# Kernel optimization log

Measured on AMD Instinct MI355X. Metric: run time of the kernel, lower is better.

## Reference

```python
import jax, jax.numpy as jnp
import numpy as np

B, NU, IN, H, VD = 4096, 6, 600, 600, 400
KD_IN, NH_IN = 64, 1
KD_C, NH_C = 32, 4
K = 4


def setup_inputs() -> dict:
    key = jax.random.key(0)
    ks = jax.random.split(key, 12)
    f = jax.random.normal
    return dict(
        x=f(ks[0], (B, 1, IN), jnp.float32),
        hs=f(ks[1], (B, NU, H), jnp.float32),
        cs=f(ks[2], (B, NU, H), jnp.float32),
        Wk=f(ks[3], (IN, NH_IN * KD_IN), jnp.float32) * 0.02,   # input-attn key Linear (no bias)
        Wv=f(ks[4], (IN, NH_IN * VD), jnp.float32) * 0.02,      # input-attn value Linear (no bias)
        Wq=f(ks[5], (NU, H, NH_IN * KD_IN), jnp.float32) * 0.01,  # GroupLinear query
        Wi2h=f(ks[6], (NU, VD, 4 * H), jnp.float32) * 0.01,     # GroupLSTMCell i2h
        Wh2h=f(ks[7], (NU, H, 4 * H), jnp.float32) * 0.01,      # GroupLSTMCell h2h
        Wck=f(ks[8], (NU, H, NH_C * KD_C), jnp.float32) * 0.01,  # comm key GroupLinear
        Wcq=f(ks[9], (NU, H, NH_C * KD_C), jnp.float32) * 0.01,  # comm query GroupLinear
        Wcv=f(ks[10], (NU, H, NH_C * H), jnp.float32) * 0.01,   # comm value GroupLinear
        Wco=f(ks[11], (NU, NH_C * H, H), jnp.float32) * 0.01,   # comm output_fc GroupLinear
    )


def _heads(t, nh, d):
    # (B, N, nh*d) -> (B, nh, N, d)
    b, n, _ = t.shape
    return t.reshape(b, n, nh, d).transpose(0, 2, 1, 3)


def reference(x, hs, cs, Wk, Wv, Wq, Wi2h, Wh2h, Wck, Wcq, Wcv, Wco):
    b = x.shape[0]
    # append null input along key axis -> (B, 2, IN)
    xcat = jnp.concatenate([x, jnp.zeros((b, 1, IN), x.dtype)], axis=1)

    # ---- input attention + top-k unit mask ----
    key = _heads(xcat @ Wk, NH_IN, KD_IN)                 # (B, nh, 2, kd)
    val = _heads(xcat @ Wv, NH_IN, VD).mean(axis=1)       # (B, 2, vd) (mean over heads)
    qry = _heads(jnp.einsum('buh,uhk->buk', hs, Wq), NH_IN, KD_IN)  # (B, nh, NU, kd)
    scores = jnp.einsum('bhuk,bhmk->bhum', qry, key) / jnp.sqrt(jnp.asarray(KD_IN, x.dtype))
    scores = scores.mean(axis=1)                          # (B, NU, 2)
    idx = jax.lax.top_k(scores[:, :, 0], K)[1]            # (B, K) active units
    mask = jnp.zeros((b, NU), x.dtype).at[jnp.arange(b)[:, None], idx].set(1.0)
    probs = jax.nn.softmax(scores, axis=-1)               # (dropout p is identity in eval)
    inputs = jnp.einsum('bum,bmv->buv', probs, val) * mask[:, :, None]  # (B, NU, vd)

    # ---- grouped LSTM cell ----
    preact = (jnp.einsum('buv,uvo->buo', inputs, Wi2h)
              + jnp.einsum('buh,uho->buo', hs, Wh2h))     # (B, NU, 4H)
    gates = jax.nn.sigmoid(preact[:, :, :3 * H])
    g_t = jnp.tanh(preact[:, :, 3 * H:])
    i_t = gates[:, :, :H]
    f_t = gates[:, :, H:2 * H]
    o_t = gates[:, :, 2 * H:]
    c_t = cs * f_t + i_t * g_t
    h_t = o_t * jnp.tanh(c_t)

    # ---- blocked_grad: identity fwd, grad*mask bwd ----
    m3 = mask[:, :, None]
    h_b = h_t * m3 + jax.lax.stop_gradient(h_t * (1.0 - m3))

    # ---- masked communication attention ----
    ck = _heads(jnp.einsum('buh,uhk->buk', h_b, Wck), NH_C, KD_C)  # (B, nh, NU, kd)
    cq = _heads(jnp.einsum('buh,uhk->buk', h_b, Wcq), NH_C, KD_C)
    cv = _heads(jnp.einsum('buh,uhk->buk', h_b, Wcv), NH_C, H)     # (B, nh, NU, H)
    cscores = jnp.einsum('bhuk,bhmk->bhum', cq, ck) / jnp.sqrt(jnp.asarray(KD_C, x.dtype))
    cprobs = jax.nn.softmax(cscores, axis=-1) * mask[:, None, :, None]  # mask query rows
    ctx = jnp.einsum('bhum,bhmd->bhud', cprobs, cv)       # (B, nh, NU, H)
    ctx = ctx.transpose(0, 2, 1, 3).reshape(b, NU, NH_C * H)
    ctx = jnp.einsum('buf,ufo->buo', ctx, Wco)            # (B, NU, H)
    h_new = ctx + h_b

    # ---- keep inactive units' old state ----
    hs_out = m3 * h_new + (1.0 - m3) * hs
    cs_out = m3 * c_t + (1.0 - m3) * cs
    return hs_out, cs_out
```

## Files before the change

kernel.cpp:

```cpp
#include <hip/hip_runtime.h>
#include <cstdint>
#include <cstddef>


typedef _Float16 f16;
typedef _Float16 f16x8 __attribute__((ext_vector_type(8)));
typedef float    f32x4 __attribute__((ext_vector_type(4)));

__device__ __forceinline__ void async16(const void* g, void* l) {
    __builtin_amdgcn_global_load_lds((const __attribute__((address_space(1))) void*)g,
                                     (__attribute__((address_space(3))) void*)l,
                                     16, 0, 0);
}

template <typename CT, int BN, int WM, int WN>
__global__ __launch_bounds__(512, 2)
void mfma_gemm2(const f16* __restrict__ A, const f16* __restrict__ W,
                CT* __restrict__ C, int K, int lda, int ldc, int Nreal,
                long sAu, long sWu, long sCu)
{
    constexpr int MI = 256 / WM / 16;
    const int gx = gridDim.x, gy = gridDim.y;
    int bid = blockIdx.x + gx * (blockIdx.y + gy * blockIdx.z);
    const int nwg = gx * gy * gridDim.z;
    if ((nwg & 7) == 0)
        bid = (bid & 7) * (nwg >> 3) + (bid >> 3);
    const int bx  = bid % gx;
    const int byz = bid / gx;
    const int by  = byz % gy;
    const int bz  = byz / gy;
    A += (long)bz * sAu;
    W += (long)bz * sWu;
    C += (long)bz * sCu;
    const int tm = bx * 256;
    const int tn = by * BN;

    __shared__ __attribute__((aligned(16))) f16 As[2][256 * 64];
    __shared__ __attribute__((aligned(16))) f16 Ws[2][BN * 64];

    const int tid  = threadIdx.x;
    const int wave = tid >> 6;
    const int lane = tid & 63;
    const int wm = (wave / WN) * (256 / WM);
    const int wn = (wave % WN) * (BN / WN);
    const int srow = lane >> 3;
    const int scol = ((lane & 7) ^ srow) * 8;
    const int mrow = lane & 15;
    const int kq   = (lane >> 4) * 8;
    const int swz  = (mrow & 7) << 3;

    f32x4 acc[MI][4] = {};

    auto stage = [&](int b, int kk) {
#pragma unroll
        for (int t = 0; t < 4; t++) {
            const int rb = t * 64 + wave * 8;
            async16(A + (long)(tm + rb + srow) * lda + (kk + scol), &As[b][rb * 64]);
        }
#pragma unroll
        for (int t = 0; t < BN / 64; t++) {
            const int rb = t * 64 + wave * 8;
            async16(W + (long)(tn + rb + srow) * K + (kk + scol), &Ws[b][rb * 64]);
        }
    };
    auto compute = [&](int b) {
#pragma unroll
        for (int c = 0; c < 2; c++) {
            const int cc = (c * 32 + kq) ^ swz;
            f16x8 aF[MI], wF[4];
#pragma unroll
            for (int i = 0; i < MI; i++)
                aF[i] = *(const f16x8*)&As[b][(wm + i * 16 + mrow) * 64 + cc];
#pragma unroll
            for (int j = 0; j < 4; j++)
                wF[j] = *(const f16x8*)&Ws[b][(wn + j * 16 + mrow) * 64 + cc];
#pragma unroll
            for (int i = 0; i < MI; i++)
#pragma unroll
                for (int j = 0; j < 4; j++)
                    acc[i][j] = __builtin_amdgcn_mfma_f32_16x16x32_f16(aF[i], wF[j], acc[i][j], 0, 0, 0);
        }
    };

    stage(0, 0);
    int bsel = 0;
    const int nk = K >> 6;
    for (int s = 0; s < nk; s++) {
        __syncthreads();
        if (s + 1 < nk) stage(bsel ^ 1, (s + 1) << 6);
        compute(bsel);
        bsel ^= 1;
    }
    const int rrow = (lane >> 4) * 4;
#pragma unroll
    for (int i = 0; i < MI; i++)
#pragma unroll
        for (int j = 0; j < 4; j++) {
            const int col = tn + wn + j * 16 + mrow;
            if (col < Nreal)
#pragma unroll
                for (int r = 0; r < 4; r++)
                    C[(long)(tm + wm + i * 16 + rrow + r) * ldc + col] = (CT)acc[i][j][r];
        }
}

template <typename CT>
__global__ __launch_bounds__(256)
void mfma_gemm(const f16* __restrict__ A, const f16* __restrict__ W,
               CT* __restrict__ C, int K, int lda, int ldc,
               long sAu, long sWu, long sCu)
{
    A += (long)blockIdx.z * sAu;
    W += (long)blockIdx.z * sWu;
    C += (long)blockIdx.z * sCu;
    const int tm = blockIdx.x * 128;
    const int tn = blockIdx.y * 128;
    __shared__ __attribute__((aligned(16))) f16 As[2][128 * 64];
    __shared__ __attribute__((aligned(16))) f16 Ws[2][128 * 64];
    const int tid  = threadIdx.x;
    const int wave = tid >> 6;
    const int lane = tid & 63;
    const int wm = (wave >> 1) * 64;
    const int wn = (wave & 1) * 64;
    const int srow = lane >> 3;
    const int scol = ((lane & 7) ^ srow) * 8;
    const int mrow = lane & 15;
    const int kq   = (lane >> 4) * 8;
    const int swz  = (mrow & 7) << 3;

    f32x4 acc[4][4] = {};

    auto stage = [&](int b, int kk) {
#pragma unroll
        for (int t = 0; t < 4; t++) {
            const int rbase = t * 32 + wave * 8;
            async16(A + (long)(tm + rbase + srow) * lda + (kk + scol), &As[b][rbase * 64]);
            async16(W + (long)(tn + rbase + srow) * K   + (kk + scol), &Ws[b][rbase * 64]);
        }
    };
    auto compute = [&](int b) {
#pragma unroll
        for (int c = 0; c < 2; c++) {
            const int cc = (c * 32 + kq) ^ swz;
            f16x8 aF[4], wF[4];
#pragma unroll
            for (int i = 0; i < 4; i++)
                aF[i] = *(const f16x8*)&As[b][(wm + i * 16 + mrow) * 64 + cc];
#pragma unroll
            for (int j = 0; j < 4; j++)
                wF[j] = *(const f16x8*)&Ws[b][(wn + j * 16 + mrow) * 64 + cc];
#pragma unroll
            for (int i = 0; i < 4; i++)
#pragma unroll
                for (int j = 0; j < 4; j++)
                    acc[i][j] = __builtin_amdgcn_mfma_f32_16x16x32_f16(aF[i], wF[j], acc[i][j], 0, 0, 0);
        }
    };

    stage(0, 0);
    int bsel = 0;
    const int nk = K >> 6;
    for (int s = 0; s < nk; s++) {
        __syncthreads();
        if (s + 1 < nk) stage(bsel ^ 1, (s + 1) << 6);
        compute(bsel);
        bsel ^= 1;
    }
    const int rrow = (lane >> 4) * 4;
#pragma unroll
    for (int i = 0; i < 4; i++)
#pragma unroll
        for (int j = 0; j < 4; j++)
#pragma unroll
            for (int r = 0; r < 4; r++)
                C[(long)(tm + wm + i * 16 + rrow + r) * ldc + (tn + wn + j * 16 + mrow)] = (CT)acc[i][j][r];
}

__global__ __launch_bounds__(256)
void sgemm_fused(const float* __restrict__ hs, const float* __restrict__ Wq,
                 const float* __restrict__ x, const float* __restrict__ Wk,
                 float* __restrict__ q, float* __restrict__ kx)
{
    const int z = blockIdx.z;
    const float* A; const float* W; float* C; int lda, ldc;
    if (z < 6) { A = hs + z * 600; W = Wq + (long)z * 38400; C = q + z * 64; lda = 3600; ldc = 384; }
    else       { A = x;            W = Wk;                   C = kx;         lda = 600;  ldc = 64;  }
    const int K = 600;
    const int tm = blockIdx.x * 64;
    __shared__ __attribute__((aligned(16))) float AsT[16][64];
    __shared__ __attribute__((aligned(16))) float Ws[16][64];
    const int t = threadIdx.x;
    const int arow = t >> 2, akc = (t & 3) * 4;
    const int wkw = t >> 4, wn = (t & 15) * 4;
    const int tx = t & 15, ty = t >> 4;

    float4 aR, wR;
    const float* Arow = A + (long)(tm + arow) * lda;
    auto loadA = [&](int kk) {
        const int k0 = kk + akc;
        const float* p = Arow + k0;
        if (k0 + 3 < K) aR = *(const float4*)p;
        else {
            aR.x = (k0 + 0 < K) ? p[0] : 0.f; aR.y = (k0 + 1 < K) ? p[1] : 0.f;
            aR.z = (k0 + 2 < K) ? p[2] : 0.f; aR.w = (k0 + 3 < K) ? p[3] : 0.f;
        }
    };
    auto loadW = [&](int kk) {
        const int k = kk + wkw;
        if (k < K) wR = *(const float4*)(W + (long)k * 64 + wn);
        else       wR = float4{0.f, 0.f, 0.f, 0.f};
    };
    loadA(0); loadW(0);
    float acc[4][4] = {{0.f}};
    const int NS = 38;
    for (int s = 0; s < NS; s++) {
        __syncthreads();
        AsT[akc + 0][arow] = aR.x; AsT[akc + 1][arow] = aR.y;
        AsT[akc + 2][arow] = aR.z; AsT[akc + 3][arow] = aR.w;
        *(float4*)&Ws[wkw][wn] = wR;
        __syncthreads();
        if (s + 1 < NS) { loadA((s + 1) * 16); loadW((s + 1) * 16); }
#pragma unroll
        for (int k = 0; k < 16; k++) {
            const float4 av = *(const float4*)&AsT[k][ty * 4];
            const float4 wv = *(const float4*)&Ws[k][tx * 4];
            acc[0][0] += av.x * wv.x; acc[0][1] += av.x * wv.y; acc[0][2] += av.x * wv.z; acc[0][3] += av.x * wv.w;
            acc[1][0] += av.y * wv.x; acc[1][1] += av.y * wv.y; acc[1][2] += av.y * wv.z; acc[1][3] += av.y * wv.w;
            acc[2][0] += av.z * wv.x; acc[2][1] += av.z * wv.y; acc[2][2] += av.z * wv.z; acc[2][3] += av.z * wv.w;
            acc[3][0] += av.w * wv.x; acc[3][1] += av.w * wv.y; acc[3][2] += av.w * wv.z; acc[3][3] += av.w * wv.w;
        }
    }
#pragma unroll
    for (int r = 0; r < 4; r++)
#pragma unroll
        for (int c = 0; c < 4; c++)
            C[(long)(tm + ty * 4 + r) * ldc + tx * 4 + c] = acc[r][c];
}

__global__ __launch_bounds__(256)
void wtrans(const float* __restrict__ src, f16* __restrict__ dst,
            int K, int N, int Kp, int Np, int ldd, long sSrc, long sDst)
{
    src += (long)blockIdx.z * sSrc;
    dst += (long)blockIdx.z * sDst;
    __shared__ float tile[32][33];
    const int tK = blockIdx.x * 32, tN = blockIdx.y * 32;
    const int tx = threadIdx.x & 31, ty = threadIdx.x >> 5;
#pragma unroll
    for (int i = 0; i < 4; i++) {
        const int k = tK + ty + i * 8, n = tN + tx;
        tile[ty + i * 8][tx] = (k < K && n < N) ? src[(long)k * N + n] : 0.f;
    }
    __syncthreads();
#pragma unroll
    for (int i = 0; i < 4; i++) {
        const int n = tN + ty + i * 8, k = tK + tx;
        if (n < Np && k < Kp) dst[(long)n * ldd + k] = (f16)tile[tx][ty + i * 8];
    }
}

__global__ void xconv_kernel(const float* __restrict__ x, f16* __restrict__ xf, long n)
{
    const long i = (long)blockIdx.x * 256 + threadIdx.x;
    if (i >= n) return;
    const long b = i / 640;
    const int c = (int)(i - b * 640);
    xf[i] = (f16)(c < 600 ? x[b * 600 + c] : 0.f);
}

__global__ void s0_kernel(const float* __restrict__ q, const float* __restrict__ kx,
                          float* __restrict__ s0, int n)
{
    const int i = blockIdx.x * 256 + threadIdx.x;
    if (i >= n) return;
    const int b = i / 6;
    const float* qp = q + (long)i * 64;
    const float* kp = kx + (long)b * 64;
    float s = 0.f;
#pragma unroll
    for (int k = 0; k < 64; k++) s += qp[k] * kp[k];
    s0[i] = s * 0.125f;
}

__global__ void mask_kernel(const float* __restrict__ s0, float* __restrict__ mask,
                            float* __restrict__ alpha, int Bc)
{
    const int b = blockIdx.x * 256 + threadIdx.x;
    if (b >= Bc) return;
    float v[6];
#pragma unroll
    for (int u = 0; u < 6; u++) v[u] = s0[b * 6 + u];
#pragma unroll
    for (int u = 0; u < 6; u++) {
        int rank = 0;
#pragma unroll
        for (int m = 0; m < 6; m++)
            rank += ((v[m] > v[u]) || (v[m] == v[u] && m < u)) ? 1 : 0;
        const float mk = (rank < 4) ? 1.f : 0.f;
        mask[b * 6 + u] = mk;
        alpha[b * 6 + u] = mk / (1.f + __expf(-v[u]));
    }
}

__global__ void inputs_kernel(const float* __restrict__ vx, const float* __restrict__ hs,
                              const float* __restrict__ alpha, f16* __restrict__ icat, long n)
{
    const long i = (long)blockIdx.x * 256 + threadIdx.x;
    if (i >= n) return;
    const int k = (int)(i & 1023);
    const long bu = i >> 10;
    float v;
    if (k < 400)       v = alpha[bu] * vx[(bu / 6) * 512 + k];
    else if (k < 1000) v = hs[bu * 600 + (k - 400)];
    else               v = 0.f;
    icat[i] = (f16)v;
}

__device__ __forceinline__ float tanh_fast(float x) {
    x = fminf(20.f, fmaxf(-20.f, x));
    const float e = __expf(2.f * x);
    return (e - 1.f) / (e + 1.f);
}

__global__ void lstm_kernel(const f16* __restrict__ pre, const float* __restrict__ cs,
                            const float* __restrict__ mask, float* __restrict__ cs_out,
                            f16* __restrict__ hbf, long n)
{
    const long i = (long)blockIdx.x * 256 + threadIdx.x;
    if (i >= n) return;
    const long bu = i / 640;
    const int h = (int)(i - bu * 640);
    if (h >= 600) { hbf[i] = (f16)0.f; return; }
    const f16* p = pre + bu * 2432;
    const float ig = 1.f / (1.f + __expf(-(float)p[h]));
    const float fg = 1.f / (1.f + __expf(-(float)p[600 + h]));
    const float og = 1.f / (1.f + __expf(-(float)p[1200 + h]));
    const float g  = tanh_fast((float)p[1800 + h]);
    const float cold = cs[bu * 600 + h];
    const float c = cold * fg + ig * g;
    cs_out[bu * 600 + h] = (mask[bu] != 0.f) ? c : cold;
    hbf[i] = (f16)(og * tanh_fast(c));
}

__global__ __launch_bounds__(256)
void attn_kernel(const f16* __restrict__ out2, const float* __restrict__ mask,
                 f16* __restrict__ ctx)
{
    const long b = blockIdx.x;
    __shared__ float sck[6][128];
    __shared__ float scq[6][128];
    __shared__ float sp[4][6][6];
    const int t = threadIdx.x;
#pragma unroll
    for (int m = 0; m < 6; m++) {
        const f16* row = out2 + (b * 6 + m) * 2688;
        if (t < 128) sck[m][t] = (float)row[2400 + t];
        else         scq[m][t - 128] = (float)row[2528 + (t - 128)];
    }
    __syncthreads();
    if (t < 144) {
        const int h = t / 36, u = (t / 6) % 6, m = t % 6;
        float s = 0.f;
#pragma unroll
        for (int k = 0; k < 32; k++) s += scq[u][h * 32 + k] * sck[m][h * 32 + k];
        sp[h][u][m] = s * 0.1767766952966369f;
    }
    __syncthreads();
    if (t < 24) {
        const int h = t / 6, u = t % 6;
        float mx = sp[h][u][0];
#pragma unroll
        for (int m = 1; m < 6; m++) mx = fmaxf(mx, sp[h][u][m]);
        float e[6], sum = 0.f;
#pragma unroll
        for (int m = 0; m < 6; m++) { e[m] = __expf(sp[h][u][m] - mx); sum += e[m]; }
        const float sc = mask[b * 6 + u] / sum;
#pragma unroll
        for (int m = 0; m < 6; m++) sp[h][u][m] = e[m] * sc;
    }
    __syncthreads();
    for (int f = t; f < 2432; f += 256) {
        if (f < 2400) {
            const int h = f / 600;
            float cv[6];
#pragma unroll
            for (int m = 0; m < 6; m++) cv[m] = (float)out2[(b * 6 + m) * 2688 + f];
#pragma unroll
            for (int u = 0; u < 6; u++) {
                float s = 0.f;
#pragma unroll
                for (int m = 0; m < 6; m++) s += sp[h][u][m] * cv[m];
                ctx[(b * 6 + u) * 2432 + f] = (f16)s;
            }
        } else {
#pragma unroll
            for (int u = 0; u < 6; u++) ctx[(b * 6 + u) * 2432 + f] = (f16)0.f;
        }
    }
}

__global__ void epi_kernel(const f16* __restrict__ ctxW, const f16* __restrict__ hbf,
                           const float* __restrict__ hs, const float* __restrict__ mask,
                           float* __restrict__ hs_out, long n)
{
    const long i = (long)blockIdx.x * 256 + threadIdx.x;
    if (i >= n) return;
    const long bu = i / 600;
    const int h = (int)(i - bu * 600);
    hs_out[i] = (mask[bu] != 0.f) ? ((float)ctxW[bu * 640 + h] + (float)hbf[bu * 640 + h]) : hs[i];
}

static inline unsigned cdivu(long a, long b) { return (unsigned)((a + b - 1) / b); }

extern "C" void kernel_launch(void* const* d_in, const int* in_sizes, int n_in,
                              void* d_out, int out_size, void* d_ws, size_t ws_size,
                              hipStream_t stream)
{
    (void)in_sizes; (void)n_in; (void)out_size;
    const float* x    = (const float*)d_in[0];
    const float* hs   = (const float*)d_in[1];
    const float* cs   = (const float*)d_in[2];
    const float* Wk   = (const float*)d_in[3];
    const float* Wv   = (const float*)d_in[4];
    const float* Wq   = (const float*)d_in[5];
    const float* Wi2h = (const float*)d_in[6];
    const float* Wh2h = (const float*)d_in[7];
    const float* Wck  = (const float*)d_in[8];
    const float* Wcq  = (const float*)d_in[9];
    const float* Wcv  = (const float*)d_in[10];
    const float* Wco  = (const float*)d_in[11];
    float* hs_out = (float*)d_out;
    float* cs_out = hs_out + (long)4096 * 6 * 600;

    char* wsb = (char*)d_ws;
    size_t off = 0;
    auto alloc = [&](size_t bytes) -> char* {
        char* p = wsb + off;
        off += (bytes + 255) & ~(size_t)255;
        return p;
    };

    f16* W1T = (f16*)alloc((size_t)6 * 2560 * 1024 * 2);
    f16* W2T = (f16*)alloc((size_t)6 * 2816 * 640 * 2);
    f16* W3T = (f16*)alloc((size_t)6 * 640 * 2432 * 2);
    f16* WvT = (f16*)alloc((size_t)512 * 640 * 2);

    f16*   xf   = (f16*)  alloc((size_t)4096 * 640 * 2);
    float* kx   = (float*)alloc((size_t)4096 * 64 * 4);
    float* vx   = (float*)alloc((size_t)4096 * 512 * 4);
    float* q    = (float*)alloc((size_t)4096 * 384 * 4);
    float* s0   = (float*)alloc((size_t)4096 * 6 * 4);
    float* alph = (float*)alloc((size_t)4096 * 6 * 4);
    float* mskv = (float*)alloc((size_t)4096 * 6 * 4);
    const size_t fixedbytes = off;

    const size_t perRow = 81408;
    int Bc = 4096;
    while (Bc > 256 && fixedbytes + (size_t)Bc * perRow + 16384 > ws_size) Bc >>= 1;

    f16* icat = (f16*)alloc((size_t)Bc * 6 * 1024 * 2);
    f16* pre  = (f16*)alloc((size_t)Bc * 6 * 2432 * 2);
    f16* hbf  = (f16*)alloc((size_t)Bc * 6 * 640 * 2);
    f16* out2 = (f16*)alloc((size_t)Bc * 6 * 2688 * 2);
    f16* ctx  = pre;
    f16* ctxW = out2;

    wtrans<<<dim3(13, 80, 6), 256, 0, stream>>>(Wi2h, W1T,        400, 2400, 400, 2560, 1024, 960000L,  2621440L);
    wtrans<<<dim3(20, 80, 6), 256, 0, stream>>>(Wh2h, W1T + 400,  600, 2400, 624, 2560, 1024, 1440000L, 2621440L);
    wtrans<<<dim3(20, 75, 6), 256, 0, stream>>>(Wcv,  W2T,        600, 2400, 640, 2400, 640,  1440000L, 1802240L);
    wtrans<<<dim3(20, 4, 6),  256, 0, stream>>>(Wck,  W2T + (long)2400 * 640, 600, 128, 640, 128, 640, 76800L, 1802240L);
    wtrans<<<dim3(20, 9, 6),  256, 0, stream>>>(Wcq,  W2T + (long)2528 * 640, 600, 128, 640, 288, 640, 76800L, 1802240L);
    wtrans<<<dim3(76, 20, 6), 256, 0, stream>>>(Wco,  W3T,        2400, 600, 2432, 640, 2432, 1440000L, 1556480L);
    wtrans<<<dim3(20, 16, 1), 256, 0, stream>>>(Wv,   WvT,        600,  400, 640, 512, 640,  0L, 0L);

    xconv_kernel<<<cdivu((long)4096 * 640, 256), 256, 0, stream>>>(x, xf, (long)4096 * 640);
    sgemm_fused<<<dim3(64, 1, 7), 256, 0, stream>>>(hs, Wq, x, Wk, q, kx);
    mfma_gemm<float><<<dim3(32, 4, 1), 256, 0, stream>>>(xf, WvT, vx, 640, 640, 512, 0, 0, 0);
    s0_kernel<<<cdivu((long)4096 * 6, 256), 256, 0, stream>>>(q, kx, s0, 4096 * 6);
    mask_kernel<<<cdivu(4096, 256), 256, 0, stream>>>(s0, mskv, alph, 4096);

    for (int b0 = 0; b0 < 4096; b0 += Bc) {
        const float* hsc = hs + (long)b0 * 3600;
        const float* csc = cs + (long)b0 * 3600;
        float* hso = hs_out + (long)b0 * 3600;
        float* cso = cs_out + (long)b0 * 3600;

        inputs_kernel<<<cdivu((long)Bc * 6144, 256), 256, 0, stream>>>(
            vx + (long)b0 * 512, hsc, alph + (long)b0 * 6, icat, (long)Bc * 6144);
        mfma_gemm2<f16, 256, 2, 4><<<dim3(Bc / 256, 10, 6), 512, 0, stream>>>(
            icat, W1T, pre, 1024, 6144, 14592, 2432, 1024, 2621440, 2432);
        lstm_kernel<<<cdivu((long)Bc * 3840, 256), 256, 0, stream>>>(
            pre, csc, mskv + (long)b0 * 6, cso, hbf, (long)Bc * 3840);
        mfma_gemm2<f16, 256, 2, 4><<<dim3(Bc / 256, 11, 6), 512, 0, stream>>>(
            hbf, W2T, out2, 640, 3840, 16128, 2688, 640, 1802240, 2688);
        attn_kernel<<<Bc, 256, 0, stream>>>(out2, mskv + (long)b0 * 6, ctx);
        mfma_gemm2<f16, 128, 4, 2><<<dim3(Bc / 256, 5, 6), 512, 0, stream>>>(
            ctx, W3T, ctxW, 2432, 14592, 3840, 640, 2432, 1556480, 640);
        epi_kernel<<<cdivu((long)Bc * 3600, 256), 256, 0, stream>>>(
            ctxW, hbf, hsc, mskv + (long)b0 * 6, hso, (long)Bc * 3600);
    }
}
```

Before: 1.030 ms.

## Add 8-wave ping-pong pipelined MFMA GEMM for LSTM and comm projections

After: 996.8 us. 3.2% less time.

```diff
diff --git a/kernel.cpp b/kernel.cpp
--- a/kernel.cpp
+++ b/kernel.cpp
@@ -11,6 +11,129 @@
     __builtin_amdgcn_global_load_lds((const __attribute__((address_space(1))) void*)g,
                                      (__attribute__((address_space(3))) void*)l,
                                      16, 0, 0);
+}
+
+__device__ __forceinline__ void BAR() { __builtin_amdgcn_s_barrier(); }
+__device__ __forceinline__ void VMW2() {
+    asm volatile("s_waitcnt vmcnt(2)" ::: "memory");
+    __builtin_amdgcn_sched_barrier(0);
+}
+__device__ __forceinline__ void VMW0() {
+    asm volatile("s_waitcnt vmcnt(0)" ::: "memory");
+    __builtin_amdgcn_sched_barrier(0);
+}
+
+template <typename CT>
+__global__ __launch_bounds__(512, 2)
+void mfma_gemm8(const f16* __restrict__ A, const f16* __restrict__ W,
+                CT* __restrict__ C, int K, int lda, int ldc, int Nreal,
+                long sAu, long sWu, long sCu)
+{
+    const int gx = gridDim.x, gy = gridDim.y;
+    int bid = blockIdx.x + gx * (blockIdx.y + gy * blockIdx.z);
+    const int nwg = gx * gy * gridDim.z;
+    if ((nwg & 7) == 0)
+        bid = (bid & 7) * (nwg >> 3) + (bid >> 3);
+    const int bx  = bid % gx;
+    const int byz = bid / gx;
+    const int by  = byz % gy;
+    const int bz  = byz / gy;
+    A += (long)bz * sAu;
+    W += (long)bz * sWu;
+    C += (long)bz * sCu;
+    const int tm = bx * 256;
+    const int tn = by * 256;
+
+    __shared__ __attribute__((aligned(16))) f16 As[2][256 * 64];
+    __shared__ __attribute__((aligned(16))) f16 Ws[2][256 * 64];
+
+    const int tid  = threadIdx.x;
+    const int wave = tid >> 6;
+    const int lane = tid & 63;
+    const int wm = (wave >> 2) * 128;
+    const int wn = (wave & 3) * 64;
+    const int srow = lane >> 3;
+    const int scol = ((lane & 7) ^ srow) * 8;
+    const int mrow = lane & 15;
+    const int kq   = (lane >> 4) * 8;
+    const int swz  = (mrow & 7) << 3;
+
+    f32x4 acc[8][4] = {};
+    f16x8 wF[4], aF[4];
+
+    auto stageH = [&](int b, int kt, int hq) {
+        const int kk = kt << 6;
+        const int rb0 = (hq & 1) * 128;
+#pragma unroll
+        for (int t2 = 0; t2 < 2; t2++) {
+            const int rb = rb0 + t2 * 64 + wave * 8;
+            if (hq < 2) async16(A + (long)(tm + rb + srow) * lda + (kk + scol), &As[b][rb * 64]);
+            else        async16(W + (long)(tn + rb + srow) * K   + (kk + scol), &Ws[b][rb * 64]);
+        }
+    };
+    auto ldW = [&](int b, int c) {
+        const int cc = (c * 32 + kq) ^ swz;
+#pragma unroll
+        for (int j = 0; j < 4; j++)
+            wF[j] = *(const f16x8*)&Ws[b][(wn + j * 16 + mrow) * 64 + cc];
+    };
+    auto ldA = [&](int b, int c, int ih) {
+        const int cc = (c * 32 + kq) ^ swz;
+#pragma unroll
+        for (int i = 0; i < 4; i++)
+            aF[i] = *(const f16x8*)&As[b][(wm + ih * 64 + i * 16 + mrow) * 64 + cc];
+    };
+    auto mma = [&](int ih) {
+        __builtin_amdgcn_s_setprio(1);
+#pragma unroll
+        for (int i = 0; i < 4; i++)
+#pragma unroll
+            for (int j = 0; j < 4; j++)
+                acc[ih * 4 + i][j] = __builtin_amdgcn_mfma_f32_16x16x32_f16(aF[i], wF[j], acc[ih * 4 + i][j], 0, 0, 0);
+        __builtin_amdgcn_s_setprio(0);
+    };
+
+    const int nk = K >> 6;
+#pragma unroll
+    for (int h = 0; h < 4; h++) stageH(0, 0, h);
+
+    for (int t = 0; t < nk; t++) {
+        const int b  = t & 1;
+        const bool pf = (t + 1 < nk);
+        if (pf) stageH(b ^ 1, t + 1, 0);
+        if (pf) VMW2(); else VMW0();
+        BAR();
+        ldW(b, 0); ldA(b, 0, 0);
+        mma(0);
+        BAR();
+        ldA(b, 0, 1);
+        if (pf) stageH(b ^ 1, t + 1, 1);
+        BAR();
+        mma(1);
+        BAR();
+        ldW(b, 1); ldA(b, 1, 0);
+        if (pf) stageH(b ^ 1, t + 1, 2);
+        BAR();
+        mma(0);
+        BAR();
+        ldA(b, 1, 1);
+        if (pf) stageH(b ^ 1, t + 1, 3);
+        BAR();
+        mma(1);
+        BAR();
+    }
+
+    const int rrow = (lane >> 4) * 4;
+#pragma unroll
+    for (int i = 0; i < 8; i++)
+#pragma unroll
+        for (int j = 0; j < 4; j++) {
+            const int col = tn + wn + j * 16 + mrow;
+            if (col < Nreal)
+#pragma unroll
+                for (int r = 0; r < 4; r++)
+                    C[(long)(tm + wm + i * 16 + rrow + r) * ldc + col] = (CT)acc[i][j][r];
+        }
 }
 
 template <typename CT, int BN, int WM, int WN>
@@ -487,11 +610,11 @@
 
         inputs_kernel<<<cdivu((long)Bc * 6144, 256), 256, 0, stream>>>(
             vx + (long)b0 * 512, hsc, alph + (long)b0 * 6, icat, (long)Bc * 6144);
-        mfma_gemm2<f16, 256, 2, 4><<<dim3(Bc / 256, 10, 6), 512, 0, stream>>>(
+        mfma_gemm8<f16><<<dim3(Bc / 256, 10, 6), 512, 0, stream>>>(
             icat, W1T, pre, 1024, 6144, 14592, 2432, 1024, 2621440, 2432);
         lstm_kernel<<<cdivu((long)Bc * 3840, 256), 256, 0, stream>>>(
             pre, csc, mskv + (long)b0 * 6, cso, hbf, (long)Bc * 3840);
-        mfma_gemm2<f16, 256, 2, 4><<<dim3(Bc / 256, 11, 6), 512, 0, stream>>>(
+        mfma_gemm8<f16><<<dim3(Bc / 256, 11, 6), 512, 0, stream>>>(
             hbf, W2T, out2, 640, 3840, 16128, 2688, 640, 1802240, 2688);
         attn_kernel<<<Bc, 256, 0, stream>>>(out2, mskv + (long)b0 * 6, ctx);
         mfma_gemm2<f16, 128, 4, 2><<<dim3(Bc / 256, 5, 6), 512, 0, stream>>>(
```
